# Performance work log

Hardware: AMD Instinct MI355X
Metric: run time of the kernel (lower is better)

## Reference

```python
import jax, jax.numpy as jnp
import numpy as np

R_FRAC = 0.5  # r_token


def setup_inputs() -> dict:
    key = jax.random.key(0)
    B, T, C = 64, 577, 1024
    hidden_states = jax.random.normal(key, (B, T, C), dtype=jnp.float32)
    return {"hidden_states": hidden_states}


def _match_indices(x, r):
    # Bipartite soft matching (class_token=True, distill_token=False).
    metric = x / jnp.linalg.norm(x, axis=-1, keepdims=True)
    a, b = metric[:, ::2, :], metric[:, 1::2, :]  # [B, Ta, C], [B, Tb, C]
    scores = jnp.einsum('bic,bjc->bij', a, b)     # [B, Ta, Tb]
    scores = scores.at[:, 0, :].set(-jnp.inf)     # protect CLS token (even index 0)
    node_max = scores.max(axis=-1)                # best sim of each src to any dst
    node_idx = scores.argmax(axis=-1)             # matched dst for each src
    edge_idx = jnp.argsort(-node_max, axis=-1)    # descending by similarity
    unm_idx = jnp.sort(edge_idx[:, r:], axis=-1)  # unmerged src (sorted: keeps CLS first)
    src_idx = edge_idx[:, :r]                     # src tokens to merge
    dst_idx = jnp.take_along_axis(node_idx, src_idx, axis=-1)
    return unm_idx, src_idx, dst_idx


def _merge_sum(v, unm_idx, src_idx, dst_idx):
    # Gather unmerged + scatter-add merged src into dst, then concat.
    src, dst = v[:, ::2, :], v[:, 1::2, :]
    unm = jnp.take_along_axis(src, unm_idx[..., None], axis=1)
    srcg = jnp.take_along_axis(src, src_idx[..., None], axis=1)
    dst = jax.vmap(lambda d, i, s: d.at[i].add(s))(dst, dst_idx, srcg)
    return jnp.concatenate([unm, dst], axis=1)


def reference(hidden_states):
    x = hidden_states
    B, T, C = x.shape
    protected = 1  # class token
    r = min(int(R_FRAC * T), (T - protected) // 2)  # 288 for T=577
    unm_idx, src_idx, dst_idx = _match_indices(x, r)
    # merge_wavg with size=None -> size = ones
    size = jnp.ones((B, T, 1), dtype=x.dtype)
    xm = _merge_sum(x * size, unm_idx, src_idx, dst_idx)
    sm = _merge_sum(size, unm_idx, src_idx, dst_idx)
    return xm / sm  # [B, T - r, C]
```

## Files before the change

kernel.cpp:

```cpp
#include <hip/hip_runtime.h>
#include <hip/hip_bf16.h>
#include <math.h>


#define B_   64
#define T_   577
#define C_   1024
#define NA   289
#define NB   288

#define EPS_MARGIN 0.08f

#define BOFF 16384

typedef __bf16 bf16x8 __attribute__((ext_vector_type(8)));
typedef float  floatx4 __attribute__((ext_vector_type(4)));

__device__ __forceinline__ unsigned int pk_bf16_trunc(unsigned int e1, unsigned int e0) {
  return __builtin_amdgcn_perm(e1, e0, 0x07060302u);
}

__device__ __forceinline__ void load16f(const float* x, size_t off, float* v) {
  const float4* p = (const float4*)(x + off);
  float4 a = p[0], b = p[1], c = p[2], d = p[3];
  v[0]=a.x; v[1]=a.y; v[2]=a.z; v[3]=a.w;
  v[4]=b.x; v[5]=b.y; v[6]=b.z; v[7]=b.w;
  v[8]=c.x; v[9]=c.y; v[10]=c.z; v[11]=c.w;
  v[12]=d.x; v[13]=d.y; v[14]=d.z; v[15]=d.w;
}

#define RNORMD_OFF 0
#define RNORMF_OFF 147456
#define DST_OFF    221184
#define S_OFF      295168

__global__ __launch_bounds__(256) void k_norms(const float* __restrict__ x,
                                               double* __restrict__ rnormd,
                                               float* __restrict__ rnormf) {
  int wid = threadIdx.x >> 6, lane = threadIdx.x & 63;
  int gw = blockIdx.x * 4 + wid;
  int b = gw / NB, j = gw - b * NB;
  float v[16];
  load16f(x, (size_t)(b * T_ + 2 * j + 1) * C_ + lane * 16, v);
  double s = 0.0;
#pragma unroll
  for (int t = 0; t < 16; ++t) s += (double)v[t] * (double)v[t];
#pragma unroll
  for (int d = 32; d >= 1; d >>= 1) s += __shfl_xor(s, d, 64);
  if (lane == 0) {
    double r = 1.0 / sqrt(s);
    rnormd[b * NB + j] = r;
    rnormf[b * NB + j] = (float)r;
  }
}

__global__ __launch_bounds__(256, 2) void k_scores(const float* __restrict__ x,
                                                   const float* __restrict__ rnormf,
                                                   float* __restrict__ S) {
  __shared__ unsigned char smem[16384 + 18432];
  int tid = threadIdx.x;
  int b  = blockIdx.x;
  int rb = blockIdx.y >> 1;
  int cb = blockIdx.y & 1;
  int wv = tid >> 6, lane = tid & 63;
  int m = lane & 15, q = lane >> 4;
  int sw = m & 7;

  floatx4 acc0[9], acc1[9];
#pragma unroll
  for (int j = 0; j < 9; ++j) { acc0[j] = (floatx4){0,0,0,0}; acc1[j] = (floatx4){0,0,0,0}; }

  const int r0 = wv * 32 + m;
  const int r1 = r0 + 16;

  for (int kc = 0; kc < 16; ++kc) {
    int k0 = kc * 64;
    __syncthreads();
    for (int v = tid; v < 2176; v += 256) {
      int isB  = v >= 1024;
      int w    = isB ? v - 1024 : v;
      int row  = w >> 3, slot = w & 7;
      int gk   = slot ^ (row & 7);
      int tok;
      if (isB) tok = 2 * (cb * 144 + row) + 1;
      else { tok = 2 * (rb * 128 + row); if (tok > 576) tok = 576; }
      const uint4* src = (const uint4*)(x + (size_t)(b * T_ + tok) * C_ + k0 + gk * 8);
      uint4 lo = src[0], hi = src[1];
      uint4 o;
      o.x = pk_bf16_trunc(lo.y, lo.x);
      o.y = pk_bf16_trunc(lo.w, lo.z);
      o.z = pk_bf16_trunc(hi.y, hi.x);
      o.w = pk_bf16_trunc(hi.w, hi.z);
      *(uint4*)(smem + (isB ? BOFF : 0) + row * 128 + slot * 16) = o;
    }
    __syncthreads();
#pragma unroll
    for (int s = 0; s < 2; ++s) {
      int slot = (s * 4 + q) ^ sw;
      bf16x8 a0 = *(const bf16x8*)(smem + r0 * 128 + slot * 16);
      bf16x8 a1 = *(const bf16x8*)(smem + r1 * 128 + slot * 16);
#pragma unroll
      for (int j = 0; j < 9; ++j) {
        bf16x8 bfrag = *(const bf16x8*)(smem + BOFF + (j * 16 + m) * 128 + slot * 16);
        acc0[j] = __builtin_amdgcn_mfma_f32_16x16x32_bf16(a0, bfrag, acc0[j], 0,0,0);
        acc1[j] = __builtin_amdgcn_mfma_f32_16x16x32_bf16(a1, bfrag, acc1[j], 0,0,0);
      }
    }
  }

  int gi_base = rb * 128 + wv * 32 + q * 4;
#pragma unroll
  for (int j = 0; j < 9; ++j) {
    int col = cb * 144 + j * 16 + m;
    float rn = rnormf[b * NB + col];
#pragma unroll
    for (int r = 0; r < 4; ++r) {
      int gi0 = gi_base + r;
      if (gi0 < NA) S[((size_t)b * NA + gi0) * NB + col] = acc0[j][r] * rn;
      int gi1 = gi0 + 16;
      if (gi1 < NA) S[((size_t)b * NA + gi1) * NB + col] = acc1[j][r] * rn;
    }
  }
}

__global__ __launch_bounds__(256) void k_argmax(const float* __restrict__ x,
                                                const double* __restrict__ rnormd,
                                                const float* __restrict__ S,
                                                int* __restrict__ dst) {
  int wid = threadIdx.x >> 6, lane = threadIdx.x & 63;
  int gw = blockIdx.x * 4 + wid;
  int b = gw / NB, i = gw - b * NB + 1;
  const float* Srow = S + ((size_t)b * NA + i) * NB;

  float sv[5]; float mx = -1e30f;
#pragma unroll
  for (int g = 0; g < 5; ++g) {
    int c = g * 64 + lane;
    sv[g] = (c < NB) ? Srow[c] : -1e30f;
    mx = fmaxf(mx, sv[g]);
  }
#pragma unroll
  for (int d = 32; d >= 1; d >>= 1) mx = fmaxf(mx, __shfl_xor(mx, d, 64));
  float thr = mx - EPS_MARGIN;

  float av[16];
  load16f(x, (size_t)(b * T_ + 2 * i) * C_ + lane * 16, av);

  double best = -1e300; int bestc = 0;
  for (int g = 0; g < 5; ++g) {
    unsigned long long mask = __ballot(sv[g] >= thr);
    while (mask) {
      int c = __ffsll((long long)mask) - 1;
      mask &= mask - 1;
      int col = g * 64 + c;
      float bv[16];
      load16f(x, (size_t)(b * T_ + 2 * col + 1) * C_ + lane * 16, bv);
      double s = 0.0;
#pragma unroll
      for (int t = 0; t < 16; ++t) s += (double)av[t] * (double)bv[t];
#pragma unroll
      for (int d = 32; d >= 1; d >>= 1) s += __shfl_xor(s, d, 64);
      s *= rnormd[b * NB + col];
      if (s > best) { best = s; bestc = col; }
    }
  }
  if (lane == 0) dst[b * NA + i] = bestc;
}

__global__ __launch_bounds__(256) void k_merge(const float* __restrict__ x,
                                               const int* __restrict__ dst,
                                               float* __restrict__ out) {
  __shared__ int dstv[NA];
  __shared__ unsigned short lists[4][292];
  __shared__ int cnts[4];
  int b = blockIdx.y, tid = threadIdx.x;
  int orow_base = blockIdx.x * 4;

  for (int i = tid; i < NA; i += 256) dstv[i] = (i >= 1) ? dst[b * NA + i] : -1;
  if (tid < 4) cnts[tid] = 0;
  __syncthreads();

  for (int i = 1 + tid; i <= 288; i += 256) {
    int d = dstv[i];
#pragma unroll
    for (int w4 = 0; w4 < 4; ++w4) {
      int orow_w = orow_base + w4;
      if (orow_w >= 1 && orow_w < NA && d == orow_w - 1) {
        int idx = atomicAdd(&cnts[w4], 1);
        lists[w4][idx] = (unsigned short)i;
      }
    }
  }
  __syncthreads();

  int wv = tid >> 6, lane = tid & 63;
  int orow = orow_base + wv;
  if (orow >= NA) return;

  const size_t xb = (size_t)b * T_ * C_;
  int c0 = lane * 16;
  float acc[16];
  float inv = 1.0f;

  if (orow == 0) {
    load16f(x, xb + c0, acc);
  } else {
    int j = orow - 1;
    load16f(x, xb + (size_t)(2 * j + 1) * C_ + c0, acc);
    int cnt = cnts[wv];
    for (int e = 0; e < cnt; ++e) {
      int i = lists[wv][e];
      float tv[16];
      load16f(x, xb + (size_t)(2 * i) * C_ + c0, tv);
#pragma unroll
      for (int t = 0; t < 16; ++t) acc[t] += tv[t];
    }
    inv = 1.0f / (float)(cnt + 1);
  }

  float4* op = (float4*)(out + ((size_t)b * NA + orow) * C_ + c0);
  op[0] = make_float4(acc[0]*inv,  acc[1]*inv,  acc[2]*inv,  acc[3]*inv);
  op[1] = make_float4(acc[4]*inv,  acc[5]*inv,  acc[6]*inv,  acc[7]*inv);
  op[2] = make_float4(acc[8]*inv,  acc[9]*inv,  acc[10]*inv, acc[11]*inv);
  op[3] = make_float4(acc[12]*inv, acc[13]*inv, acc[14]*inv, acc[15]*inv);
}

extern "C" void kernel_launch(void* const* d_in, const int* in_sizes, int n_in,
                              void* d_out, int out_size, void* d_ws, size_t ws_size,
                              hipStream_t stream) {
  const float* x = (const float*)d_in[0];
  float* out     = (float*)d_out;
  char* ws = (char*)d_ws;
  double* rnormd = (double*)(ws + RNORMD_OFF);
  float*  rnormf = (float*)(ws + RNORMF_OFF);
  int*    dst    = (int*)(ws + DST_OFF);
  float*  S      = (float*)(ws + S_OFF);

  k_norms <<<B_ * NB / 4, 256, 0, stream>>>(x, rnormd, rnormf);
  k_scores<<<dim3(B_, 6), 256, 0, stream>>>(x, rnormf, S);
  k_argmax<<<B_ * NB / 4, 256, 0, stream>>>(x, rnormd, S, dst);
  k_merge <<<dim3((NA + 3) / 4, B_), 256, 0, stream>>>(x, dst, out);
}
```

Before: 353.8 us.

## Fuse norms and row argmax into score GEMM epilogue, drop full score matrix

Removes the separate norm kernel and the full fp32 score matrix write and read. The score kernel now computes column sums of squares in shared memory during the tile load, and takes the per-row max through a packed 64-bit score and column key in the epilogue. It also retiles to 96x96 blocks with a 3x3 MFMA fragment grid per wave. Near-tie candidates within a smaller margin are kept in a capped extras list, and a recheck kernel re-scores them in fp64. The risks are a narrower margin and a capped candidate list, which could change argmax ties, plus atomics and an added memset.

New measurement: 341.5 us. 3.5% less time.

```diff
diff --git a/kernel.cpp b/kernel.cpp
--- a/kernel.cpp
+++ b/kernel.cpp
@@ -1,5 +1,4 @@
 #include <hip/hip_runtime.h>
-#include <hip/hip_bf16.h>
 #include <math.h>
 
 
@@ -8,13 +7,45 @@
 #define C_   1024
 #define NA   289
 #define NB   288
-
-#define EPS_MARGIN 0.08f
-
-#define BOFF 16384
+#define EPS_MARGIN 0.04f
+
+#define RPAD 384
+#define EXTRA_CAP 12
 
 typedef __bf16 bf16x8 __attribute__((ext_vector_type(8)));
 typedef float  floatx4 __attribute__((ext_vector_type(4)));
+typedef unsigned long long u64;
+
+#define ECNT_OFF   0
+#define GRPWIN_OFF 98304
+#define EXTRA_OFF  (GRPWIN_OFF + 1179648)
+#define DST_OFF    (EXTRA_OFF + 2359296)
+
+__device__ __forceinline__ u64 shfl_xor_u64(u64 v, int msk) {
+  unsigned int lo = (unsigned int)v, hi = (unsigned int)(v >> 32);
+  lo = __shfl_xor(lo, msk, 64);
+  hi = __shfl_xor(hi, msk, 64);
+  return ((u64)hi << 32) | (u64)lo;
+}
+__device__ __forceinline__ double shfl_xor_f64(double v, int msk) {
+  u64 u = __double_as_longlong(v);
+  return __longlong_as_double((long long)shfl_xor_u64(u, msk));
+}
+
+__device__ __forceinline__ unsigned int fkey(float s) {
+  unsigned int fb = __float_as_uint(s);
+  return (fb & 0x80000000u) ? ~fb : (fb | 0x80000000u);
+}
+__device__ __forceinline__ float keyf(unsigned int k) {
+  return (k & 0x80000000u) ? __uint_as_float(k ^ 0x80000000u) : __uint_as_float(~k);
+}
+__device__ __forceinline__ u64 packsc(float s, int col) {
+  return ((u64)fkey(s) << 32) | (u64)(0xFFFFFFFFu - (unsigned int)col);
+}
+__device__ __forceinline__ int pcol(u64 p) {
+  return (int)(0xFFFFFFFFu - (unsigned int)(p & 0xFFFFFFFFull));
+}
+__device__ __forceinline__ float pscore(u64 p) { return keyf((unsigned int)(p >> 32)); }
 
 __device__ __forceinline__ unsigned int pk_bf16_trunc(unsigned int e1, unsigned int e0) {
   return __builtin_amdgcn_perm(e1, e0, 0x07060302u);
@@ -29,61 +60,42 @@
   v[12]=d.x; v[13]=d.y; v[14]=d.z; v[15]=d.w;
 }
 
-#define RNORMD_OFF 0
-#define RNORMF_OFF 147456
-#define DST_OFF    221184
-#define S_OFF      295168
-
-__global__ __launch_bounds__(256) void k_norms(const float* __restrict__ x,
-                                               double* __restrict__ rnormd,
-                                               float* __restrict__ rnormf) {
-  int wid = threadIdx.x >> 6, lane = threadIdx.x & 63;
-  int gw = blockIdx.x * 4 + wid;
-  int b = gw / NB, j = gw - b * NB;
-  float v[16];
-  load16f(x, (size_t)(b * T_ + 2 * j + 1) * C_ + lane * 16, v);
-  double s = 0.0;
-#pragma unroll
-  for (int t = 0; t < 16; ++t) s += (double)v[t] * (double)v[t];
-#pragma unroll
-  for (int d = 32; d >= 1; d >>= 1) s += __shfl_xor(s, d, 64);
-  if (lane == 0) {
-    double r = 1.0 / sqrt(s);
-    rnormd[b * NB + j] = r;
-    rnormf[b * NB + j] = (float)r;
-  }
-}
-
 __global__ __launch_bounds__(256, 2) void k_scores(const float* __restrict__ x,
-                                                   const float* __restrict__ rnormf,
-                                                   float* __restrict__ S) {
-  __shared__ unsigned char smem[16384 + 18432];
+                                                   u64* __restrict__ grpwin,
+                                                   unsigned int* __restrict__ ecnt,
+                                                   u64* __restrict__ extras) {
+  __shared__ unsigned char smem[24576];
+  __shared__ float sumsq[96];
   int tid = threadIdx.x;
   int b  = blockIdx.x;
-  int rb = blockIdx.y >> 1;
-  int cb = blockIdx.y & 1;
+  int rt = blockIdx.y;
+  int ct = blockIdx.z;
   int wv = tid >> 6, lane = tid & 63;
   int m = lane & 15, q = lane >> 4;
   int sw = m & 7;
 
-  floatx4 acc0[9], acc1[9];
-#pragma unroll
-  for (int j = 0; j < 9; ++j) { acc0[j] = (floatx4){0,0,0,0}; acc1[j] = (floatx4){0,0,0,0}; }
-
-  const int r0 = wv * 32 + m;
-  const int r1 = r0 + 16;
+  if (tid < 96) sumsq[tid] = 0.f;
+
+  floatx4 acc[3][3];
+#pragma unroll
+  for (int ii = 0; ii < 3; ++ii)
+#pragma unroll
+    for (int jj = 0; jj < 3; ++jj) acc[ii][jj] = (floatx4){0,0,0,0};
+
+  const int ib = (wv >> 1) * 3;
+  const int jb = (wv & 1) * 3;
 
   for (int kc = 0; kc < 16; ++kc) {
     int k0 = kc * 64;
     __syncthreads();
-    for (int v = tid; v < 2176; v += 256) {
-      int isB  = v >= 1024;
-      int w    = isB ? v - 1024 : v;
+    for (int v = tid; v < 1536; v += 256) {
+      int isB  = v >= 768;
+      int w    = isB ? v - 768 : v;
       int row  = w >> 3, slot = w & 7;
       int gk   = slot ^ (row & 7);
       int tok;
-      if (isB) tok = 2 * (cb * 144 + row) + 1;
-      else { tok = 2 * (rb * 128 + row); if (tok > 576) tok = 576; }
+      if (isB) tok = 2 * (ct * 96 + row) + 1;
+      else { tok = 2 * (rt * 96 + row); if (tok > 576) tok = 576; }
       const uint4* src = (const uint4*)(x + (size_t)(b * T_ + tok) * C_ + k0 + gk * 8);
       uint4 lo = src[0], hi = src[1];
       uint4 o;
@@ -91,80 +103,137 @@
       o.y = pk_bf16_trunc(lo.w, lo.z);
       o.z = pk_bf16_trunc(hi.y, hi.x);
       o.w = pk_bf16_trunc(hi.w, hi.z);
-      *(uint4*)(smem + (isB ? BOFF : 0) + row * 128 + slot * 16) = o;
+      *(uint4*)(smem + (isB ? 12288 : 0) + row * 128 + slot * 16) = o;
+      if (isB) {
+        float f0 = __uint_as_float(lo.x), f1 = __uint_as_float(lo.y);
+        float f2 = __uint_as_float(lo.z), f3 = __uint_as_float(lo.w);
+        float f4 = __uint_as_float(hi.x), f5 = __uint_as_float(hi.y);
+        float f6 = __uint_as_float(hi.z), f7 = __uint_as_float(hi.w);
+        float ss = f0*f0 + f1*f1 + f2*f2 + f3*f3 + f4*f4 + f5*f5 + f6*f6 + f7*f7;
+        atomicAdd(&sumsq[row], ss);
+      }
     }
     __syncthreads();
 #pragma unroll
     for (int s = 0; s < 2; ++s) {
       int slot = (s * 4 + q) ^ sw;
-      bf16x8 a0 = *(const bf16x8*)(smem + r0 * 128 + slot * 16);
-      bf16x8 a1 = *(const bf16x8*)(smem + r1 * 128 + slot * 16);
-#pragma unroll
-      for (int j = 0; j < 9; ++j) {
-        bf16x8 bfrag = *(const bf16x8*)(smem + BOFF + (j * 16 + m) * 128 + slot * 16);
-        acc0[j] = __builtin_amdgcn_mfma_f32_16x16x32_bf16(a0, bfrag, acc0[j], 0,0,0);
-        acc1[j] = __builtin_amdgcn_mfma_f32_16x16x32_bf16(a1, bfrag, acc1[j], 0,0,0);
-      }
-    }
-  }
-
-  int gi_base = rb * 128 + wv * 32 + q * 4;
-#pragma unroll
-  for (int j = 0; j < 9; ++j) {
-    int col = cb * 144 + j * 16 + m;
-    float rn = rnormf[b * NB + col];
+      bf16x8 af[3], bf[3];
+#pragma unroll
+      for (int ii = 0; ii < 3; ++ii)
+        af[ii] = *(const bf16x8*)(smem + ((ib + ii) * 16 + m) * 128 + slot * 16);
+#pragma unroll
+      for (int jj = 0; jj < 3; ++jj)
+        bf[jj] = *(const bf16x8*)(smem + 12288 + ((jb + jj) * 16 + m) * 128 + slot * 16);
+#pragma unroll
+      for (int ii = 0; ii < 3; ++ii)
+#pragma unroll
+        for (int jj = 0; jj < 3; ++jj)
+          acc[ii][jj] = __builtin_amdgcn_mfma_f32_16x16x32_bf16(af[ii], bf[jj], acc[ii][jj], 0,0,0);
+    }
+  }
+
+  float rn[3];
+#pragma unroll
+  for (int jj = 0; jj < 3; ++jj) rn[jj] = rsqrtf(sumsq[(jb + jj) * 16 + m]);
+
+  int g = ct * 2 + (wv & 1);
+#pragma unroll
+  for (int ii = 0; ii < 3; ++ii) {
 #pragma unroll
     for (int r = 0; r < 4; ++r) {
-      int gi0 = gi_base + r;
-      if (gi0 < NA) S[((size_t)b * NA + gi0) * NB + col] = acc0[j][r] * rn;
-      int gi1 = gi0 + 16;
-      if (gi1 < NA) S[((size_t)b * NA + gi1) * NB + col] = acc1[j][r] * rn;
-    }
-  }
-}
-
-__global__ __launch_bounds__(256) void k_argmax(const float* __restrict__ x,
-                                                const double* __restrict__ rnormd,
-                                                const float* __restrict__ S,
-                                                int* __restrict__ dst) {
+      u64 pj[3];
+#pragma unroll
+      for (int jj = 0; jj < 3; ++jj) {
+        float s = acc[ii][jj][r] * rn[jj];
+        pj[jj] = packsc(s, ct * 96 + (jb + jj) * 16 + m);
+      }
+      u64 pk = pj[0];
+      if (pj[1] > pk) pk = pj[1];
+      if (pj[2] > pk) pk = pj[2];
+#pragma unroll
+      for (int d = 1; d < 16; d <<= 1) {
+        u64 o = shfl_xor_u64(pk, d);
+        if (o > pk) pk = o;
+      }
+      int grow = rt * 96 + (ib + ii) * 16 + q * 4 + r;
+      float thr = pscore(pk) - EPS_MARGIN;
+      size_t rbase = (size_t)b * RPAD + grow;
+#pragma unroll
+      for (int jj = 0; jj < 3; ++jj) {
+        if (pj[jj] != pk && pscore(pj[jj]) >= thr) {
+          unsigned int idx = atomicAdd(&ecnt[rbase], 1u);
+          if (idx < EXTRA_CAP) extras[rbase * EXTRA_CAP + idx] = pj[jj];
+        }
+      }
+      if (m == 0) grpwin[rbase * 6 + g] = pk;
+    }
+  }
+}
+
+__global__ __launch_bounds__(256) void k_recheck(const float* __restrict__ x,
+                                                 const u64* __restrict__ grpwin,
+                                                 const unsigned int* __restrict__ ecnt,
+                                                 const u64* __restrict__ extras,
+                                                 int* __restrict__ dst) {
   int wid = threadIdx.x >> 6, lane = threadIdx.x & 63;
   int gw = blockIdx.x * 4 + wid;
   int b = gw / NB, i = gw - b * NB + 1;
-  const float* Srow = S + ((size_t)b * NA + i) * NB;
-
-  float sv[5]; float mx = -1e30f;
-#pragma unroll
-  for (int g = 0; g < 5; ++g) {
-    int c = g * 64 + lane;
-    sv[g] = (c < NB) ? Srow[c] : -1e30f;
-    mx = fmaxf(mx, sv[g]);
-  }
-#pragma unroll
-  for (int d = 32; d >= 1; d >>= 1) mx = fmaxf(mx, __shfl_xor(mx, d, 64));
-  float thr = mx - EPS_MARGIN;
-
-  float av[16];
-  load16f(x, (size_t)(b * T_ + 2 * i) * C_ + lane * 16, av);
-
-  double best = -1e300; int bestc = 0;
-  for (int g = 0; g < 5; ++g) {
-    unsigned long long mask = __ballot(sv[g] >= thr);
-    while (mask) {
-      int c = __ffsll((long long)mask) - 1;
-      mask &= mask - 1;
-      int col = g * 64 + c;
+  size_t rbase = (size_t)b * RPAD + i;
+
+  u64 v = (lane < 6) ? grpwin[rbase * 6 + lane] : 0ull;
+#pragma unroll
+  for (int d = 1; d < 8; d <<= 1) {
+    u64 o = shfl_xor_u64(v, d);
+    if (o > v) v = o;
+  }
+  v = shfl_xor_u64(v, 0) , v = v;
+  {
+    unsigned int lo = (unsigned int)v, hi = (unsigned int)(v >> 32);
+    lo = __shfl(lo, 0, 64); hi = __shfl(hi, 0, 64);
+    v = ((u64)hi << 32) | lo;
+  }
+  float thr = pscore(v) - EPS_MARGIN;
+
+  u64 cand[14]; int nc = 0;
+#pragma unroll
+  for (int t = 0; t < 6; ++t) {
+    u64 w = grpwin[rbase * 6 + t];
+    if (pscore(w) >= thr && nc < 14) cand[nc++] = w;
+  }
+  unsigned int ec = ecnt[rbase]; if (ec > EXTRA_CAP) ec = EXTRA_CAP;
+  for (unsigned int t = 0; t < ec; ++t) {
+    u64 w = extras[rbase * EXTRA_CAP + t];
+    if (pscore(w) >= thr && nc < 14) cand[nc++] = w;
+  }
+
+  int best;
+  if (nc <= 1) {
+    best = pcol(v);
+  } else {
+    float av[16];
+    load16f(x, (size_t)(b * T_ + 2 * i) * C_ + lane * 16, av);
+    double bs = -1e300; int bc = 1 << 30;
+    for (int c = 0; c < nc; ++c) {
+      int col = pcol(cand[c]);
       float bv[16];
       load16f(x, (size_t)(b * T_ + 2 * col + 1) * C_ + lane * 16, bv);
-      double s = 0.0;
-#pragma unroll
-      for (int t = 0; t < 16; ++t) s += (double)av[t] * (double)bv[t];
-#pragma unroll
-      for (int d = 32; d >= 1; d >>= 1) s += __shfl_xor(s, d, 64);
-      s *= rnormd[b * NB + col];
-      if (s > best) { best = s; bestc = col; }
-    }
-  }
-  if (lane == 0) dst[b * NA + i] = bestc;
+      double dot = 0.0, nsq = 0.0;
+#pragma unroll
+      for (int t = 0; t < 16; ++t) {
+        dot += (double)av[t] * (double)bv[t];
+        nsq += (double)bv[t] * (double)bv[t];
+      }
+#pragma unroll
+      for (int d = 32; d >= 1; d >>= 1) {
+        dot += shfl_xor_f64(dot, d);
+        nsq += shfl_xor_f64(nsq, d);
+      }
+      double s = dot / sqrt(nsq);
+      if (s > bs || (s == bs && col < bc)) { bs = s; bc = col; }
+    }
+    best = bc;
+  }
+  if (lane == 0) dst[b * NA + i] = best;
 }
 
 __global__ __launch_bounds__(256) void k_merge(const float* __restrict__ x,
@@ -231,13 +300,13 @@
   const float* x = (const float*)d_in[0];
   float* out     = (float*)d_out;
   char* ws = (char*)d_ws;
-  double* rnormd = (double*)(ws + RNORMD_OFF);
-  float*  rnormf = (float*)(ws + RNORMF_OFF);
-  int*    dst    = (int*)(ws + DST_OFF);
-  float*  S      = (float*)(ws + S_OFF);
-
-  k_norms <<<B_ * NB / 4, 256, 0, stream>>>(x, rnormd, rnormf);
-  k_scores<<<dim3(B_, 6), 256, 0, stream>>>(x, rnormf, S);
-  k_argmax<<<B_ * NB / 4, 256, 0, stream>>>(x, rnormd, S, dst);
-  k_merge <<<dim3((NA + 3) / 4, B_), 256, 0, stream>>>(x, dst, out);
-}
+  unsigned int* ecnt = (unsigned int*)(ws + ECNT_OFF);
+  u64* grpwin        = (u64*)(ws + GRPWIN_OFF);
+  u64* extras        = (u64*)(ws + EXTRA_OFF);
+  int* dst           = (int*)(ws + DST_OFF);
+
+  hipMemsetAsync(ecnt, 0, (size_t)B_ * RPAD * sizeof(unsigned int), stream);
+  k_scores <<<dim3(B_, 4, 3), 256, 0, stream>>>(x, grpwin, ecnt, extras);
+  k_recheck<<<B_ * NB / 4, 256, 0, stream>>>(x, grpwin, ecnt, extras, dst);
+  k_merge  <<<dim3((NA + 3) / 4, B_), 256, 0, stream>>>(x, dst, out);
+}
```
